# Optimization experiments

Measured on AMD Instinct MI355X. Metric: run time of the kernel, lower is better.

## Reference

```python
import jax, jax.numpy as jnp
import numpy as np

STEPS, BATCH = 2048, 512
INPUT_DIM = 16          # climate features after stripping flow channel
STORE_DIM = 8           # number of conceptual stores S
HIDDEN = 128
SLOW = 2                # SLOW_STORE index
RAIN_IDX = 0            # rain column within sliced climate inputs
OUT_DIM = STORE_DIM * (STORE_DIM + 2)   # flow_between_stores=True -> 80
IN_DIM_FLOWNET = INPUT_DIM + STORE_DIM  # 24


def setup_inputs() -> dict:
    key = jax.random.key(0)
    ks = jax.random.split(key, 10)
    hyd_input = jax.random.uniform(ks[0], (STEPS, BATCH, 1 + INPUT_DIM), dtype=jnp.float32)
    s = 0.05
    W0 = jax.random.normal(ks[1], (HIDDEN, IN_DIM_FLOWNET), dtype=jnp.float32) * s
    b0 = jax.random.normal(ks[2], (HIDDEN,), dtype=jnp.float32) * s
    W1 = jax.random.normal(ks[3], (HIDDEN, HIDDEN), dtype=jnp.float32) * s
    b1 = jax.random.normal(ks[4], (HIDDEN,), dtype=jnp.float32) * s
    W_in = jax.random.normal(ks[5], (STORE_DIM + 1, HIDDEN), dtype=jnp.float32) * s
    b_in = jax.random.normal(ks[6], (STORE_DIM + 1,), dtype=jnp.float32) * s
    W_out = jax.random.normal(ks[7], (OUT_DIM, HIDDEN), dtype=jnp.float32) * s
    b_out = jax.random.normal(ks[8], (OUT_DIM,), dtype=jnp.float32) * s - 3.0  # bias.data -= 3
    return {"hyd_input": hyd_input, "W0": W0, "b0": b0, "W1": W1, "b1": b1,
            "W_in": W_in, "b_in": b_in, "W_out": W_out, "b_out": b_out}


def reference(hyd_input, W0, b0, W1, b1, W_in, b_in, W_out, b_out):
    S = STORE_DIM
    flow = hyd_input[:, :, 0]          # [T, B] observed flow
    x = hyd_input[:, :, 1:]            # [T, B, F] climate forcings
    rain = x[:, :, RAIN_IDX]           # [T, B]
    # correct_init_baseflow: 25th percentile of observed flow over time, per batch elem
    baseflow = jnp.percentile(flow, 25.0, axis=0)  # [B]

    B = x.shape[1]
    stores0 = jnp.zeros((B, S), dtype=hyd_input.dtype).at[:, 1].set(1.0)  # init_stores

    def step(stores, inp):
        x_t, rain_t, is_first = inp
        # flownet: (num_layers=2) Linear -> ReLU (dropout is eval-mode identity)
        h = jnp.concatenate([x_t, 0.01 * stores], axis=1)      # [B, F+S]
        h = jax.nn.relu(h @ W0.T + b0)
        h = jax.nn.relu(h @ W1.T + b1)
        # inflow gating (softmax over S+1): distribute rain into stores
        a = jax.nn.softmax(h @ W_in.T + b_in, axis=-1)          # [B, S+1]
        stores = stores + a[:, 1:] * rain_t[:, None]
        # outflow fluxes (sigmoid), S*(S+2) = inter-store | escape | flow
        b = jax.nn.sigmoid(h @ W_out.T + b_out)                 # [B, S*(S+2)]
        # sequential inter-store transfers (order matters; S is small/fixed)
        for d in range(S):
            fb = b[:, d * S:(d + 1) * S] * stores               # [B, S]
            stores = (stores - fb).at[:, d].add(fb.sum(axis=1))
        escape = b[:, -2 * S:-S] * stores
        stores = stores - escape
        b_flow = b[:, -S:]
        flow_distn = b_flow * stores
        stores = stores - flow_distn
        # at i==0: overwrite slow store from baseflow / outflow coeff
        corrected = stores.at[:, SLOW].set(baseflow / jnp.maximum(b_flow[:, SLOW], 1e-5))
        stores = jnp.where(is_first, corrected, stores)
        return stores, flow_distn.sum(axis=1)

    is_first = jnp.arange(x.shape[0]) == 0
    _, flows = jax.lax.scan(step, stores0, (x, rain, is_first))
    return flows  # [T, B]
```

## Files before the change

### kernel.cpp

```cpp
#include <hip/hip_runtime.h>
#include <hip/hip_bf16.h>
#include <math.h>

#define STEPS 2048
#define BATCH 512

typedef __attribute__((ext_vector_type(8))) short short8;
typedef __attribute__((ext_vector_type(4))) short short4v;
typedef __attribute__((ext_vector_type(2))) short short2v;
typedef __attribute__((ext_vector_type(4))) float f32x4;
typedef __attribute__((ext_vector_type(2))) float f32x2;

__device__ __forceinline__ short f2bf(float f) {
    union { float f; unsigned u; } v; v.f = f;
    unsigned u = v.u;
    return (short)((u + 0x7FFFu + ((u >> 16) & 1u)) >> 16);
}
__device__ __forceinline__ short2v pk2(float a, float b) {
    __hip_bfloat162 h = __float22bfloat162_rn(make_float2(a, b));
    union { __hip_bfloat162 h; short2v s; } u; u.h = h; return u.s;
}

__global__ __launch_bounds__(256) void baseflow_kernel(
    const float* __restrict__ hyd, float* __restrict__ bf)
{
    __shared__ float arr[STEPS];
    const int b = blockIdx.x;
    const int tid = threadIdx.x;
    for (int t = tid; t < STEPS; t += 256)
        arr[t] = hyd[(size_t)(t * BATCH + b) * 17];
    __syncthreads();
    for (int k = 2; k <= STEPS; k <<= 1) {
        for (int j = k >> 1; j > 0; j >>= 1) {
            for (int i = tid; i < STEPS; i += 256) {
                int ixj = i ^ j;
                if (ixj > i) {
                    float a = arr[i], c = arr[ixj];
                    bool up = ((i & k) == 0);
                    if (up ? (a > c) : (a < c)) { arr[i] = c; arr[ixj] = a; }
                }
            }
            __syncthreads();
        }
    }
    if (tid == 0) bf[b] = arr[511] + 0.75f * (arr[512] - arr[511]);
}

__global__ __launch_bounds__(256, 1) void hyd_step_kernel(
    const float* __restrict__ hyd,
    const float* __restrict__ W0,  const float* __restrict__ b0,
    const float* __restrict__ W1,  const float* __restrict__ b1,
    const float* __restrict__ Win, const float* __restrict__ bin,
    const float* __restrict__ Wout,const float* __restrict__ bout,
    const float* __restrict__ baseflow,
    float* __restrict__ out)
{
    __shared__ __align__(16) short h1F[256 * 8];
    __shared__ __align__(16) short h2F[256 * 8];
    __shared__ __align__(16) float hb[2][100];

    const int tid  = threadIdx.x;
    const int blk  = blockIdx.x;
    const int lane = tid & 63;
    const int wv   = tid >> 6;
    const int cn   = lane & 15;
    const int cg   = lane >> 4;
    const int col  = lane & 1;

    for (int i = tid; i < 256 * 8; i += 256) { h1F[i] = 0; h2F[i] = 0; }

    short8 a0[2]; f32x4 c0[2];
    short8 a1[2][4]; f32x4 c1[2];
    short8 ah[2][4]; f32x4 ch[2];
    #pragma unroll
    for (int i = 0; i < 2; ++i) {
        const int mt = 2 * wv + i;
        const int row = mt * 16 + cn;
        #pragma unroll
        for (int j = 0; j < 8; ++j) {
            int k = cg * 8 + j;
            a0[i][j] = (k < 24) ? f2bf(W0[row * 24 + k]) : (short)0;
        }
        #pragma unroll
        for (int kt = 0; kt < 4; ++kt)
            #pragma unroll
            for (int j = 0; j < 8; ++j)
                a1[i][kt][j] = f2bf(W1[row * 128 + kt * 32 + cg * 8 + j]);
        #pragma unroll
        for (int r = 0; r < 4; ++r) {
            int m = mt * 16 + cg * 4 + r;
            c0[i][r] = b0[m];
            c1[i][r] = b1[m];
        }
    }
    const int nht = (wv < 2) ? 2 : 1;
    int htile[2];
    htile[0] = (wv < 2) ? 2 * wv : 4 + (wv - 2);
    htile[1] = (wv < 2) ? 2 * wv + 1 : htile[0];
    #pragma unroll
    for (int i = 0; i < 2; ++i) {
        const int ht = htile[i];
        const int row = ht * 16 + cn;
        #pragma unroll
        for (int kt = 0; kt < 4; ++kt)
            #pragma unroll
            for (int j = 0; j < 8; ++j) {
                int k = kt * 32 + cg * 8 + j;
                float w = 0.f;
                if (row != 1) {
                    int q = (row == 0) ? 0 : (row - 1);
                    if (q < 9)       w = Win[q * 128 + k];
                    else if (q < 89) w = Wout[(q - 9) * 128 + k];
                }
                ah[i][kt][j] = f2bf(w);
            }
        #pragma unroll
        for (int r = 0; r < 4; ++r) {
            int m = ht * 16 + cg * 4 + r;
            float bb = 0.f;
            if (m != 1) {
                int q = (m == 0) ? 0 : (m - 1);
                if (q < 9)       bb = bin[q];
                else if (q < 89) bb = bout[q - 9];
            }
            ch[i][r] = bb;
        }
    }

    f32x2 s01 = {0.f, 1.f}, s23 = {0.f, 0.f}, s45 = {0.f, 0.f}, s67 = {0.f, 0.f};
    const float bfv = baseflow[blk * 2 + col];
    short8 spack;
    {
        short2v p0 = pk2(0.01f * s01.x, 0.01f * s01.y);
        short2v p1 = pk2(0.01f * s23.x, 0.01f * s23.y);
        short2v p2 = pk2(0.01f * s45.x, 0.01f * s45.y);
        short2v p3 = pk2(0.01f * s67.x, 0.01f * s67.y);
        spack[0] = p0[0]; spack[1] = p0[1]; spack[2] = p1[0]; spack[3] = p1[1];
        spack[4] = p2[0]; spack[5] = p2[1]; spack[6] = p3[0]; spack[7] = p3[1];
    }

    const bool xlane = (cn < 2) && (cg < 2);
    const int xoff = (blk * 2 + cn) * 17 + 1 + cg * 8;
    const int roff = (blk * 2 + col) * 17 + 1;
    float xv[8];
    float rain_next;
    if (xlane) {
        const float* p = hyd + xoff;
        #pragma unroll
        for (int j = 0; j < 8; ++j) xv[j] = p[j];
    }
    rain_next = hyd[roff];

    f32x4 accx0, accx1;
    {
        short8 xfrag = 0;
        if (xlane) {
            short2v q0 = pk2(xv[0], xv[1]), q1 = pk2(xv[2], xv[3]),
                    q2 = pk2(xv[4], xv[5]), q3 = pk2(xv[6], xv[7]);
            xfrag[0] = q0[0]; xfrag[1] = q0[1]; xfrag[2] = q1[0]; xfrag[3] = q1[1];
            xfrag[4] = q2[0]; xfrag[5] = q2[1]; xfrag[6] = q3[0]; xfrag[7] = q3[1];
        }
        accx0 = __builtin_amdgcn_mfma_f32_16x16x32_bf16(a0[0], xfrag, c0[0], 0, 0, 0);
        accx1 = __builtin_amdgcn_mfma_f32_16x16x32_bf16(a0[1], xfrag, c0[1], 0, 0, 0);
    }

    __syncthreads();

    for (int t = 0; t < STEPS; ++t) {
        const float rain = rain_next;
        const int tn = (t + 1 < STEPS) ? (t + 1) : t;
        const float* px = hyd + (size_t)tn * (BATCH * 17);
        if (xlane) {
            const float* p = px + xoff;
            #pragma unroll
            for (int j = 0; j < 8; ++j) xv[j] = p[j];
        }
        rain_next = px[roff];

        short8 sfrag = 0;
        if (cn < 2 && cg == 2) sfrag = spack;
        #pragma unroll
        for (int i = 0; i < 2; ++i) {
            f32x4 acc = __builtin_amdgcn_mfma_f32_16x16x32_bf16(
                a0[i], sfrag, (i ? accx1 : accx0), 0, 0, 0);
            if (cn < 2) {
                int m0 = (2 * wv + i) * 16 + cg * 4;
                short4v p;
                short2v pa = pk2(fmaxf(acc[0], 0.f), fmaxf(acc[1], 0.f));
                short2v pb = pk2(fmaxf(acc[2], 0.f), fmaxf(acc[3], 0.f));
                p[0] = pa[0]; p[1] = pa[1]; p[2] = pb[0]; p[3] = pb[1];
                *(short4v*)&h1F[((m0 >> 3) * 16 + cn) * 8 + (m0 & 7)] = p;
            }
        }
        __syncthreads();

        short8 bf1[4];
        #pragma unroll
        for (int kt = 0; kt < 4; ++kt)
            bf1[kt] = *(const short8*)&h1F[(kt * 64 + lane) * 8];
        #pragma unroll
        for (int i = 0; i < 2; ++i) {
            f32x4 acc = c1[i];
            #pragma unroll
            for (int kt = 0; kt < 4; ++kt)
                acc = __builtin_amdgcn_mfma_f32_16x16x32_bf16(a1[i][kt], bf1[kt], acc, 0, 0, 0);
            if (cn < 2) {
                int m0 = (2 * wv + i) * 16 + cg * 4;
                short4v p;
                short2v pa = pk2(fmaxf(acc[0], 0.f), fmaxf(acc[1], 0.f));
                short2v pb = pk2(fmaxf(acc[2], 0.f), fmaxf(acc[3], 0.f));
                p[0] = pa[0]; p[1] = pa[1]; p[2] = pb[0]; p[3] = pb[1];
                *(short4v*)&h2F[((m0 >> 3) * 16 + cn) * 8 + (m0 & 7)] = p;
            }
        }
        __syncthreads();

        short8 bf2[4];
        #pragma unroll
        for (int kt = 0; kt < 4; ++kt)
            bf2[kt] = *(const short8*)&h2F[(kt * 64 + lane) * 8];
        #pragma unroll
        for (int i = 0; i < 2; ++i) {
            if (i < nht) {
                f32x4 acc = ch[i];
                #pragma unroll
                for (int kt = 0; kt < 4; ++kt)
                    acc = __builtin_amdgcn_mfma_f32_16x16x32_bf16(ah[i][kt], bf2[kt], acc, 0, 0, 0);
                if (cn < 2) {
                    const int ht = htile[i];
                    float4 o;
                    #pragma unroll
                    for (int r = 0; r < 4; ++r) {
                        int m = ht * 16 + cg * 4 + r;
                        float v = acc[r];
                        bool isl = (m < 10);
                        float em = __expf(isl ? v : -v);
                        float res = isl ? em : __builtin_amdgcn_rcpf(1.f + em);
                        ((float*)&o)[r] = res;
                    }
                    *(float4*)&hb[cn][ht * 16 + cg * 4] = o;
                }
            }
        }
        __syncthreads();

        float4 gq[23];
        {
            const float4* hp = (const float4*)&hb[col][0];
            #pragma unroll
            for (int c2 = 0; c2 < 23; ++c2) gq[c2] = hp[c2];
        }

        {
            short8 xfrag = 0;
            if (xlane) {
                short2v q0 = pk2(xv[0], xv[1]), q1 = pk2(xv[2], xv[3]),
                        q2 = pk2(xv[4], xv[5]), q3 = pk2(xv[6], xv[7]);
                xfrag[0] = q0[0]; xfrag[1] = q0[1]; xfrag[2] = q1[0]; xfrag[3] = q1[1];
                xfrag[4] = q2[0]; xfrag[5] = q2[1]; xfrag[6] = q3[0]; xfrag[7] = q3[1];
            }
            accx0 = __builtin_amdgcn_mfma_f32_16x16x32_bf16(a0[0], xfrag, c0[0], 0, 0, 0);
            accx1 = __builtin_amdgcn_mfma_f32_16x16x32_bf16(a0[1], xfrag, c0[1], 0, 0, 0);
        }

        {
            const f32x2* g2 = (const f32x2*)gq;
            const float* gv = (const float*)gq;

            f32x2 dt = (g2[1] + g2[2]) + (g2[3] + g2[4]);
            float den = gv[0] + dt.x + dt.y;
            float rr = rain * __builtin_amdgcn_rcpf(den);
            f32x2 rr2 = {rr, rr};
            s01 += g2[1] * rr2; s23 += g2[2] * rr2;
            s45 += g2[3] * rr2; s67 += g2[4] * rr2;

            #pragma unroll
            for (int d = 0; d < 8; ++d) {
                const int gb = 5 + 4 * d;
                f32x2 fb0 = g2[gb + 0] * s01, fb1 = g2[gb + 1] * s23;
                f32x2 fb2 = g2[gb + 2] * s45, fb3 = g2[gb + 3] * s67;
                f32x2 tt = (fb0 + fb1) + (fb2 + fb3);
                float fs = tt.x + tt.y;
                s01 -= fb0; s23 -= fb1; s45 -= fb2; s67 -= fb3;
                if      (d == 0) s01.x += fs;
                else if (d == 1) s01.y += fs;
                else if (d == 2) s23.x += fs;
                else if (d == 3) s23.y += fs;
                else if (d == 4) s45.x += fs;
                else if (d == 5) s45.y += fs;
                else if (d == 6) s67.x += fs;
                else             s67.y += fs;
            }
            s01 -= g2[37] * s01; s23 -= g2[38] * s23;
            s45 -= g2[39] * s45; s67 -= g2[40] * s67;
            f32x2 f0 = g2[41] * s01, f1 = g2[42] * s23;
            f32x2 f2 = g2[43] * s45, f3 = g2[44] * s67;
            f32x2 ft = (f0 + f1) + (f2 + f3);
            float fsum = ft.x + ft.y;
            s01 -= f0; s23 -= f1; s45 -= f2; s67 -= f3;
            if (t == 0) s23.x = bfv / fmaxf(gv[84], 1e-5f);

            {
                short2v p0 = pk2(0.01f * s01.x, 0.01f * s01.y);
                short2v p1 = pk2(0.01f * s23.x, 0.01f * s23.y);
                short2v p2 = pk2(0.01f * s45.x, 0.01f * s45.y);
                short2v p3 = pk2(0.01f * s67.x, 0.01f * s67.y);
                spack[0] = p0[0]; spack[1] = p0[1]; spack[2] = p1[0]; spack[3] = p1[1];
                spack[4] = p2[0]; spack[5] = p2[1]; spack[6] = p3[0]; spack[7] = p3[1];
            }
            if (tid < 2) out[(size_t)t * BATCH + blk * 2 + tid] = fsum;
        }
    }
}

extern "C" void kernel_launch(void* const* d_in, const int* in_sizes, int n_in,
                              void* d_out, int out_size, void* d_ws, size_t ws_size,
                              hipStream_t stream)
{
    const float* hyd  = (const float*)d_in[0];
    const float* W0   = (const float*)d_in[1];
    const float* b0   = (const float*)d_in[2];
    const float* W1   = (const float*)d_in[3];
    const float* b1   = (const float*)d_in[4];
    const float* Win  = (const float*)d_in[5];
    const float* bin  = (const float*)d_in[6];
    const float* Wout = (const float*)d_in[7];
    const float* bout = (const float*)d_in[8];
    float* out = (float*)d_out;
    float* bf  = (float*)d_ws;

    baseflow_kernel<<<BATCH, 256, 0, stream>>>(hyd, bf);
    hyd_step_kernel<<<BATCH / 2, 256, 0, stream>>>(
        hyd, W0, b0, W1, b1, Win, bin, Wout, bout, bf, out);
}
```

Baseline: 3.072 ms.

## Collapse recurrent step kernel to a single wavefront, dropping block barriers

The per-step MLP work for two batch elements moves from four wavefronts into one 64-lane wavefront that holds all weight fragments in registers. This removes the four __syncthreads per timestep, leaving only lgkmcnt waits on LDS. Biases move into LDS and are reloaded each step. The recurrent store update is split so its first half overlaps the second half's LDS loads. The cost is one wave doing all the MFMAs serially and much higher register pressure (all W1 and head tiles in VGPRs), which risks spills.

```diff
diff --git a/kernel.cpp b/kernel.cpp
--- a/kernel.cpp
+++ b/kernel.cpp
@@ -20,6 +20,9 @@
     __hip_bfloat162 h = __float22bfloat162_rn(make_float2(a, b));
     union { __hip_bfloat162 h; short2v s; } u; u.h = h; return u.s;
 }
+
+#define LGKM0()    asm volatile("s_waitcnt lgkmcnt(0)" ::: "memory")
+#define MEMFENCE() asm volatile("" ::: "memory")
 
 __global__ __launch_bounds__(256) void baseflow_kernel(
     const float* __restrict__ hyd, float* __restrict__ bf)
@@ -46,7 +49,7 @@
     if (tid == 0) bf[b] = arr[511] + 0.75f * (arr[512] - arr[511]);
 }
 
-__global__ __launch_bounds__(256, 1) void hyd_step_kernel(
+__global__ __launch_bounds__(64, 1) void hyd_step_kernel(
     const float* __restrict__ hyd,
     const float* __restrict__ W0,  const float* __restrict__ b0,
     const float* __restrict__ W1,  const float* __restrict__ b1,
@@ -55,76 +58,64 @@
     const float* __restrict__ baseflow,
     float* __restrict__ out)
 {
-    __shared__ __align__(16) short h1F[256 * 8];
-    __shared__ __align__(16) short h2F[256 * 8];
+    __shared__ __align__(16) short h1F[16 * 16 * 8];
+    __shared__ __align__(16) short h2F[16 * 16 * 8];
     __shared__ __align__(16) float hb[2][100];
-
-    const int tid  = threadIdx.x;
+    __shared__ __align__(16) float c0L[128];
+    __shared__ __align__(16) float c1L[128];
+    __shared__ __align__(16) float chL[96];
+
+    const int lane = threadIdx.x & 63;
     const int blk  = blockIdx.x;
-    const int lane = tid & 63;
-    const int wv   = tid >> 6;
     const int cn   = lane & 15;
     const int cg   = lane >> 4;
     const int col  = lane & 1;
 
-    for (int i = tid; i < 256 * 8; i += 256) { h1F[i] = 0; h2F[i] = 0; }
-
-    short8 a0[2]; f32x4 c0[2];
-    short8 a1[2][4]; f32x4 c1[2];
-    short8 ah[2][4]; f32x4 ch[2];
+    for (int i = lane; i < 16 * 16 * 8; i += 64) { h1F[i] = 0; h2F[i] = 0; }
+    for (int i = lane; i < 128; i += 64) { c0L[i] = b0[i]; c1L[i] = b1[i]; }
+    for (int i = lane; i < 96; i += 64) {
+        float v = 0.f;
+        if (i != 1) {
+            int q = (i == 0) ? 0 : (i - 1);
+            if (q < 9)       v = bin[q];
+            else if (q < 89) v = bout[q - 9];
+        }
+        chL[i] = v;
+    }
+
+    short8 a0[8];
+    short8 a1[8][4];
+    short8 ah[6][4];
     #pragma unroll
-    for (int i = 0; i < 2; ++i) {
-        const int mt = 2 * wv + i;
+    for (int mt = 0; mt < 8; ++mt) {
         const int row = mt * 16 + cn;
         #pragma unroll
         for (int j = 0; j < 8; ++j) {
             int k = cg * 8 + j;
-            a0[i][j] = (k < 24) ? f2bf(W0[row * 24 + k]) : (short)0;
+            a0[mt][j] = (k < 24) ? f2bf(W0[row * 24 + k]) : (short)0;
         }
         #pragma unroll
         for (int kt = 0; kt < 4; ++kt)
             #pragma unroll
             for (int j = 0; j < 8; ++j)
-                a1[i][kt][j] = f2bf(W1[row * 128 + kt * 32 + cg * 8 + j]);
-        #pragma unroll
-        for (int r = 0; r < 4; ++r) {
-            int m = mt * 16 + cg * 4 + r;
-            c0[i][r] = b0[m];
-            c1[i][r] = b1[m];
-        }
-    }
-    const int nht = (wv < 2) ? 2 : 1;
-    int htile[2];
-    htile[0] = (wv < 2) ? 2 * wv : 4 + (wv - 2);
-    htile[1] = (wv < 2) ? 2 * wv + 1 : htile[0];
+                a1[mt][kt][j] = f2bf(W1[row * 128 + kt * 32 + cg * 8 + j]);
+    }
     #pragma unroll
-    for (int i = 0; i < 2; ++i) {
-        const int ht = htile[i];
-        const int row = ht * 16 + cn;
+    for (int ht = 0; ht < 6; ++ht) {
+        const int p = ht * 16 + cn;
         #pragma unroll
         for (int kt = 0; kt < 4; ++kt)
             #pragma unroll
             for (int j = 0; j < 8; ++j) {
                 int k = kt * 32 + cg * 8 + j;
                 float w = 0.f;
-                if (row != 1) {
-                    int q = (row == 0) ? 0 : (row - 1);
+                if (p != 1) {
+                    int q = (p == 0) ? 0 : (p - 1);
                     if (q < 9)       w = Win[q * 128 + k];
                     else if (q < 89) w = Wout[(q - 9) * 128 + k];
                 }
-                ah[i][kt][j] = f2bf(w);
-            }
-        #pragma unroll
-        for (int r = 0; r < 4; ++r) {
-            int m = ht * 16 + cg * 4 + r;
-            float bb = 0.f;
-            if (m != 1) {
-                int q = (m == 0) ? 0 : (m - 1);
-                if (q < 9)       bb = bin[q];
-                else if (q < 89) bb = bout[q - 9];
-            }
-            ch[i][r] = bb;
-        }
+                ah[ht][kt][j] = f2bf(w);
+            }
     }
 
     f32x2 s01 = {0.f, 1.f}, s23 = {0.f, 0.f}, s45 = {0.f, 0.f}, s67 = {0.f, 0.f};
@@ -151,7 +142,11 @@
     }
     rain_next = hyd[roff];
 
-    f32x4 accx0, accx1;
+    const int wbase = ((cg >> 1) * 16 + cn) * 8 + (cg & 1) * 4;
+
+    LGKM0();
+
+    f32x4 accx[8];
     {
         short8 xfrag = 0;
         if (xlane) {
@@ -160,11 +155,12 @@
             xfrag[0] = q0[0]; xfrag[1] = q0[1]; xfrag[2] = q1[0]; xfrag[3] = q1[1];
             xfrag[4] = q2[0]; xfrag[5] = q2[1]; xfrag[6] = q3[0]; xfrag[7] = q3[1];
         }
-        accx0 = __builtin_amdgcn_mfma_f32_16x16x32_bf16(a0[0], xfrag, c0[0], 0, 0, 0);
-        accx1 = __builtin_amdgcn_mfma_f32_16x16x32_bf16(a0[1], xfrag, c0[1], 0, 0, 0);
-    }
-
-    __syncthreads();
+        #pragma unroll
+        for (int mt = 0; mt < 8; ++mt) {
+            f32x4 c0v = *(const f32x4*)&c0L[mt * 16 + cg * 4];
+            accx[mt] = __builtin_amdgcn_mfma_f32_16x16x32_bf16(a0[mt], xfrag, c0v, 0, 0, 0);
+        }
+    }
 
     for (int t = 0; t < STEPS; ++t) {
         const float rain = rain_next;
@@ -180,77 +176,83 @@
         short8 sfrag = 0;
         if (cn < 2 && cg == 2) sfrag = spack;
         #pragma unroll
-        for (int i = 0; i < 2; ++i) {
-            f32x4 acc = __builtin_amdgcn_mfma_f32_16x16x32_bf16(
-                a0[i], sfrag, (i ? accx1 : accx0), 0, 0, 0);
+        for (int mt = 0; mt < 8; ++mt) {
+            f32x4 acc = __builtin_amdgcn_mfma_f32_16x16x32_bf16(a0[mt], sfrag, accx[mt], 0, 0, 0);
             if (cn < 2) {
-                int m0 = (2 * wv + i) * 16 + cg * 4;
                 short4v p;
                 short2v pa = pk2(fmaxf(acc[0], 0.f), fmaxf(acc[1], 0.f));
                 short2v pb = pk2(fmaxf(acc[2], 0.f), fmaxf(acc[3], 0.f));
                 p[0] = pa[0]; p[1] = pa[1]; p[2] = pb[0]; p[3] = pb[1];
-                *(short4v*)&h1F[((m0 >> 3) * 16 + cn) * 8 + (m0 & 7)] = p;
-            }
-        }
-        __syncthreads();
+                *(short4v*)&h1F[wbase + mt * 256] = p;
+            }
+        }
+        f32x4 c1v[8];
+        #pragma unroll
+        for (int mt = 0; mt < 8; ++mt)
+            c1v[mt] = *(const f32x4*)&c1L[mt * 16 + cg * 4];
+        LGKM0();
 
         short8 bf1[4];
         #pragma unroll
         for (int kt = 0; kt < 4; ++kt)
             bf1[kt] = *(const short8*)&h1F[(kt * 64 + lane) * 8];
-        #pragma unroll
-        for (int i = 0; i < 2; ++i) {
-            f32x4 acc = c1[i];
+        f32x4 chv[6];
+        #pragma unroll
+        for (int ht = 0; ht < 6; ++ht)
+            chv[ht] = *(const f32x4*)&chL[ht * 16 + cg * 4];
+        #pragma unroll
+        for (int mt = 0; mt < 8; ++mt) {
+            f32x4 acc = c1v[mt];
             #pragma unroll
             for (int kt = 0; kt < 4; ++kt)
-                acc = __builtin_amdgcn_mfma_f32_16x16x32_bf16(a1[i][kt], bf1[kt], acc, 0, 0, 0);
+                acc = __builtin_amdgcn_mfma_f32_16x16x32_bf16(a1[mt][kt], bf1[kt], acc, 0, 0, 0);
             if (cn < 2) {
-                int m0 = (2 * wv + i) * 16 + cg * 4;
                 short4v p;
                 short2v pa = pk2(fmaxf(acc[0], 0.f), fmaxf(acc[1], 0.f));
                 short2v pb = pk2(fmaxf(acc[2], 0.f), fmaxf(acc[3], 0.f));
                 p[0] = pa[0]; p[1] = pa[1]; p[2] = pb[0]; p[3] = pb[1];
-                *(short4v*)&h2F[((m0 >> 3) * 16 + cn) * 8 + (m0 & 7)] = p;
-            }
-        }
-        __syncthreads();
+                *(short4v*)&h2F[wbase + mt * 256] = p;
+            }
+        }
+        LGKM0();
 
         short8 bf2[4];
         #pragma unroll
         for (int kt = 0; kt < 4; ++kt)
             bf2[kt] = *(const short8*)&h2F[(kt * 64 + lane) * 8];
         #pragma unroll
-        for (int i = 0; i < 2; ++i) {
-            if (i < nht) {
-                f32x4 acc = ch[i];
-                #pragma unroll
-                for (int kt = 0; kt < 4; ++kt)
-                    acc = __builtin_amdgcn_mfma_f32_16x16x32_bf16(ah[i][kt], bf2[kt], acc, 0, 0, 0);
-                if (cn < 2) {
-                    const int ht = htile[i];
-                    float4 o;
+        for (int ht = 0; ht < 6; ++ht) {
+            f32x4 acc = chv[ht];
+            #pragma unroll
+            for (int kt = 0; kt < 4; ++kt)
+                acc = __builtin_amdgcn_mfma_f32_16x16x32_bf16(ah[ht][kt], bf2[kt], acc, 0, 0, 0);
+            if (cn < 2) {
+                f32x4 o;
+                if (ht == 0) {
                     #pragma unroll
                     for (int r = 0; r < 4; ++r) {
-                        int m = ht * 16 + cg * 4 + r;
+                        int m = cg * 4 + r;
                         float v = acc[r];
                         bool isl = (m < 10);
                         float em = __expf(isl ? v : -v);
-                        float res = isl ? em : __builtin_amdgcn_rcpf(1.f + em);
-                        ((float*)&o)[r] = res;
+                        o[r] = isl ? em : __builtin_amdgcn_rcpf(1.f + em);
                     }
-                    *(float4*)&hb[cn][ht * 16 + cg * 4] = o;
+                } else {
+                    #pragma unroll
+                    for (int r = 0; r < 4; ++r) {
+                        float em = __expf(-acc[r]);
+                        o[r] = __builtin_amdgcn_rcpf(1.f + em);
+                    }
                 }
-            }
-        }
-        __syncthreads();
-
-        float4 gq[23];
-        {
-            const float4* hp = (const float4*)&hb[col][0];
-            #pragma unroll
-            for (int c2 = 0; c2 < 23; ++c2) gq[c2] = hp[c2];
-        }
-
+                *(f32x4*)&hb[cn][ht * 16 + cg * 4] = o;
+            }
+        }
+        LGKM0();
+
+        f32x4 gqA[11];
+        #pragma unroll
+        for (int c2 = 0; c2 < 11; ++c2)
+            gqA[c2] = *(const f32x4*)&hb[col][c2 * 4];
         {
             short8 xfrag = 0;
             if (xlane) {
@@ -259,46 +261,68 @@
                 xfrag[0] = q0[0]; xfrag[1] = q0[1]; xfrag[2] = q1[0]; xfrag[3] = q1[1];
                 xfrag[4] = q2[0]; xfrag[5] = q2[1]; xfrag[6] = q3[0]; xfrag[7] = q3[1];
             }
-            accx0 = __builtin_amdgcn_mfma_f32_16x16x32_bf16(a0[0], xfrag, c0[0], 0, 0, 0);
-            accx1 = __builtin_amdgcn_mfma_f32_16x16x32_bf16(a0[1], xfrag, c0[1], 0, 0, 0);
-        }
-
+            #pragma unroll
+            for (int mt = 0; mt < 8; ++mt) {
+                f32x4 c0v = *(const f32x4*)&c0L[mt * 16 + cg * 4];
+                accx[mt] = __builtin_amdgcn_mfma_f32_16x16x32_bf16(a0[mt], xfrag, c0v, 0, 0, 0);
+            }
+        }
+
+        const float* gvA = (const float*)gqA;
+        const f32x2* gA2 = (const f32x2*)gqA;
         {
-            const f32x2* g2 = (const f32x2*)gq;
-            const float* gv = (const float*)gq;
-
-            f32x2 dt = (g2[1] + g2[2]) + (g2[3] + g2[4]);
-            float den = gv[0] + dt.x + dt.y;
+            f32x2 dt = (gA2[1] + gA2[2]) + (gA2[3] + gA2[4]);
+            float den = gvA[0] + dt.x + dt.y;
             float rr = rain * __builtin_amdgcn_rcpf(den);
             f32x2 rr2 = {rr, rr};
-            s01 += g2[1] * rr2; s23 += g2[2] * rr2;
-            s45 += g2[3] * rr2; s67 += g2[4] * rr2;
-
-            #pragma unroll
-            for (int d = 0; d < 8; ++d) {
+            s01 += gA2[1] * rr2; s23 += gA2[2] * rr2;
+            s45 += gA2[3] * rr2; s67 += gA2[4] * rr2;
+
+            #pragma unroll
+            for (int d = 0; d < 4; ++d) {
                 const int gb = 5 + 4 * d;
-                f32x2 fb0 = g2[gb + 0] * s01, fb1 = g2[gb + 1] * s23;
-                f32x2 fb2 = g2[gb + 2] * s45, fb3 = g2[gb + 3] * s67;
+                f32x2 fb0 = gA2[gb + 0] * s01, fb1 = gA2[gb + 1] * s23;
+                f32x2 fb2 = gA2[gb + 2] * s45, fb3 = gA2[gb + 3] * s67;
                 f32x2 tt = (fb0 + fb1) + (fb2 + fb3);
                 float fs = tt.x + tt.y;
                 s01 -= fb0; s23 -= fb1; s45 -= fb2; s67 -= fb3;
                 if      (d == 0) s01.x += fs;
                 else if (d == 1) s01.y += fs;
                 else if (d == 2) s23.x += fs;
-                else if (d == 3) s23.y += fs;
-                else if (d == 4) s45.x += fs;
+                else             s23.y += fs;
+            }
+        }
+
+        MEMFENCE();
+
+        f32x4 gqB[13];
+        #pragma unroll
+        for (int c2 = 0; c2 < 13; ++c2)
+            gqB[c2] = *(const f32x4*)&hb[col][40 + c2 * 4];
+        const float* gvB = (const float*)gqB;
+        const f32x2* gB2 = (const f32x2*)gqB;
+        {
+            #pragma unroll
+            for (int d = 4; d < 8; ++d) {
+                const int gb = 4 * d - 15;
+                f32x2 fb0 = gB2[gb + 0] * s01, fb1 = gB2[gb + 1] * s23;
+                f32x2 fb2 = gB2[gb + 2] * s45, fb3 = gB2[gb + 3] * s67;
+                f32x2 tt = (fb0 + fb1) + (fb2 + fb3);
+                float fs = tt.x + tt.y;
+                s01 -= fb0; s23 -= fb1; s45 -= fb2; s67 -= fb3;
+                if      (d == 4) s45.x += fs;
                 else if (d == 5) s45.y += fs;
                 else if (d == 6) s67.x += fs;
                 else             s67.y += fs;
             }
-            s01 -= g2[37] * s01; s23 -= g2[38] * s23;
-            s45 -= g2[39] * s45; s67 -= g2[40] * s67;
-            f32x2 f0 = g2[41] * s01, f1 = g2[42] * s23;
-            f32x2 f2 = g2[43] * s45, f3 = g2[44] * s67;
+            s01 -= gB2[17] * s01; s23 -= gB2[18] * s23;
+            s45 -= gB2[19] * s45; s67 -= gB2[20] * s67;
+            f32x2 f0 = gB2[21] * s01, f1 = gB2[22] * s23;
+            f32x2 f2 = gB2[23] * s45, f3 = gB2[24] * s67;
             f32x2 ft = (f0 + f1) + (f2 + f3);
             float fsum = ft.x + ft.y;
             s01 -= f0; s23 -= f1; s45 -= f2; s67 -= f3;
-            if (t == 0) s23.x = bfv / fmaxf(gv[84], 1e-5f);
+            if (t == 0) s23.x = bfv / fmaxf(gvB[44], 1e-5f);
 
             {
                 short2v p0 = pk2(0.01f * s01.x, 0.01f * s01.y);
@@ -308,7 +332,7 @@
                 spack[0] = p0[0]; spack[1] = p0[1]; spack[2] = p1[0]; spack[3] = p1[1];
                 spack[4] = p2[0]; spack[5] = p2[1]; spack[6] = p3[0]; spack[7] = p3[1];
             }
-            if (tid < 2) out[(size_t)t * BATCH + blk * 2 + tid] = fsum;
+            if (lane < 2) out[(size_t)t * BATCH + blk * 2 + lane] = fsum;
         }
     }
 }
@@ -330,6 +354,6 @@
     float* bf  = (float*)d_ws;
 
     baseflow_kernel<<<BATCH, 256, 0, stream>>>(hyd, bf);
-    hyd_step_kernel<<<BATCH / 2, 256, 0, stream>>>(
+    hyd_step_kernel<<<BATCH / 2, 64, 0, stream>>>(
         hyd, W0, b0, W1, b1, Win, bin, Wout, bout, bf, out);
 }
```

New measurement: 5.538 ms. +80.3%, slower.

## Use LDS-only barriers, split MFMA accumulation chains, and stage gate loads

Applied to the files above, without the earlier changes.

Replaces __syncthreads with a barrier that waits only on LDS counters, so the global prefetch of the next step's inputs is not drained at each barrier. The dependent 4-MFMA accumulation chains are split into two independent pairs that are summed afterwards, which shortens MFMA latency chains. Gate values are loaded from LDS in two batches, interleaved with the first half of the store-transfer loop, and the sigmoid/exp branch is specialised by tile. This lowers register pressure and latency, but a barrier that skips vmcnt could be fragile if any global memory ordering were relied upon.

```diff
diff --git a/kernel.cpp b/kernel.cpp
--- a/kernel.cpp
+++ b/kernel.cpp
@@ -20,6 +20,10 @@
     __hip_bfloat162 h = __float22bfloat162_rn(make_float2(a, b));
     union { __hip_bfloat162 h; short2v s; } u; u.h = h; return u.s;
 }
+
+#define LBAR() do { asm volatile("s_waitcnt lgkmcnt(0)" ::: "memory"); \
+                    __builtin_amdgcn_s_barrier();                      \
+                    asm volatile("" ::: "memory"); } while (0)
 
 __global__ __launch_bounds__(256) void baseflow_kernel(
     const float* __restrict__ hyd, float* __restrict__ bf)
@@ -164,8 +168,6 @@
         accx1 = __builtin_amdgcn_mfma_f32_16x16x32_bf16(a0[1], xfrag, c0[1], 0, 0, 0);
     }
 
-    __syncthreads();
-
     for (int t = 0; t < STEPS; ++t) {
         const float rain = rain_next;
         const int tn = (t + 1 < STEPS) ? (t + 1) : t;
@@ -192,7 +194,7 @@
                 *(short4v*)&h1F[((m0 >> 3) * 16 + cn) * 8 + (m0 & 7)] = p;
             }
         }
-        __syncthreads();
+        LBAR();
 
         short8 bf1[4];
         #pragma unroll
@@ -200,10 +202,12 @@
             bf1[kt] = *(const short8*)&h1F[(kt * 64 + lane) * 8];
         #pragma unroll
         for (int i = 0; i < 2; ++i) {
-            f32x4 acc = c1[i];
-            #pragma unroll
-            for (int kt = 0; kt < 4; ++kt)
-                acc = __builtin_amdgcn_mfma_f32_16x16x32_bf16(a1[i][kt], bf1[kt], acc, 0, 0, 0);
+            f32x4 zz = {0.f, 0.f, 0.f, 0.f};
+            f32x4 accA = __builtin_amdgcn_mfma_f32_16x16x32_bf16(a1[i][0], bf1[0], c1[i], 0, 0, 0);
+            accA = __builtin_amdgcn_mfma_f32_16x16x32_bf16(a1[i][1], bf1[1], accA, 0, 0, 0);
+            f32x4 accB = __builtin_amdgcn_mfma_f32_16x16x32_bf16(a1[i][2], bf1[2], zz, 0, 0, 0);
+            accB = __builtin_amdgcn_mfma_f32_16x16x32_bf16(a1[i][3], bf1[3], accB, 0, 0, 0);
+            f32x4 acc = accA + accB;
             if (cn < 2) {
                 int m0 = (2 * wv + i) * 16 + cg * 4;
                 short4v p;
@@ -213,7 +217,7 @@
                 *(short4v*)&h2F[((m0 >> 3) * 16 + cn) * 8 + (m0 & 7)] = p;
             }
         }
-        __syncthreads();
+        LBAR();
 
         short8 bf2[4];
         #pragma unroll
@@ -222,35 +226,41 @@
         #pragma unroll
         for (int i = 0; i < 2; ++i) {
             if (i < nht) {
-                f32x4 acc = ch[i];
-                #pragma unroll
-                for (int kt = 0; kt < 4; ++kt)
-                    acc = __builtin_amdgcn_mfma_f32_16x16x32_bf16(ah[i][kt], bf2[kt], acc, 0, 0, 0);
+                f32x4 zz = {0.f, 0.f, 0.f, 0.f};
+                f32x4 accA = __builtin_amdgcn_mfma_f32_16x16x32_bf16(ah[i][0], bf2[0], ch[i], 0, 0, 0);
+                accA = __builtin_amdgcn_mfma_f32_16x16x32_bf16(ah[i][1], bf2[1], accA, 0, 0, 0);
+                f32x4 accB = __builtin_amdgcn_mfma_f32_16x16x32_bf16(ah[i][2], bf2[2], zz, 0, 0, 0);
+                accB = __builtin_amdgcn_mfma_f32_16x16x32_bf16(ah[i][3], bf2[3], accB, 0, 0, 0);
+                f32x4 acc = accA + accB;
                 if (cn < 2) {
                     const int ht = htile[i];
-                    float4 o;
-                    #pragma unroll
-                    for (int r = 0; r < 4; ++r) {
-                        int m = ht * 16 + cg * 4 + r;
-                        float v = acc[r];
-                        bool isl = (m < 10);
-                        float em = __expf(isl ? v : -v);
-                        float res = isl ? em : __builtin_amdgcn_rcpf(1.f + em);
-                        ((float*)&o)[r] = res;
+                    f32x4 o;
+                    if (ht == 0) {
+                        #pragma unroll
+                        for (int r = 0; r < 4; ++r) {
+                            int m = cg * 4 + r;
+                            float v = acc[r];
+                            bool isl = (m < 10);
+                            float em = __expf(isl ? v : -v);
+                            o[r] = isl ? em : __builtin_amdgcn_rcpf(1.f + em);
+                        }
+                    } else {
+                        #pragma unroll
+                        for (int r = 0; r < 4; ++r) {
+                            float em = __expf(-acc[r]);
+                            o[r] = __builtin_amdgcn_rcpf(1.f + em);
+                        }
                     }
-                    *(float4*)&hb[cn][ht * 16 + cg * 4] = o;
+                    *(f32x4*)&hb[cn][ht * 16 + cg * 4] = o;
                 }
             }
         }
-        __syncthreads();
-
-        float4 gq[23];
-        {
-            const float4* hp = (const float4*)&hb[col][0];
-            #pragma unroll
-            for (int c2 = 0; c2 < 23; ++c2) gq[c2] = hp[c2];
-        }
-
+        LBAR();
+
+        f32x4 gqA[11];
+        #pragma unroll
+        for (int c2 = 0; c2 < 11; ++c2)
+            gqA[c2] = *(const f32x4*)&hb[col][c2 * 4];
         {
             short8 xfrag = 0;
             if (xlane) {
@@ -263,42 +273,59 @@
             accx1 = __builtin_amdgcn_mfma_f32_16x16x32_bf16(a0[1], xfrag, c0[1], 0, 0, 0);
         }
 
+        const float* gvA = (const float*)gqA;
+        const f32x2* gA2 = (const f32x2*)gqA;
         {
-            const f32x2* g2 = (const f32x2*)gq;
-            const float* gv = (const float*)gq;
-
-            f32x2 dt = (g2[1] + g2[2]) + (g2[3] + g2[4]);
-            float den = gv[0] + dt.x + dt.y;
+            f32x2 dt = (gA2[1] + gA2[2]) + (gA2[3] + gA2[4]);
+            float den = gvA[0] + dt.x + dt.y;
             float rr = rain * __builtin_amdgcn_rcpf(den);
             f32x2 rr2 = {rr, rr};
-            s01 += g2[1] * rr2; s23 += g2[2] * rr2;
-            s45 += g2[3] * rr2; s67 += g2[4] * rr2;
-
-            #pragma unroll
-            for (int d = 0; d < 8; ++d) {
+            s01 += gA2[1] * rr2; s23 += gA2[2] * rr2;
+            s45 += gA2[3] * rr2; s67 += gA2[4] * rr2;
+
+            #pragma unroll
+            for (int d = 0; d < 4; ++d) {
                 const int gb = 5 + 4 * d;
-                f32x2 fb0 = g2[gb + 0] * s01, fb1 = g2[gb + 1] * s23;
-                f32x2 fb2 = g2[gb + 2] * s45, fb3 = g2[gb + 3] * s67;
+                f32x2 fb0 = gA2[gb + 0] * s01, fb1 = gA2[gb + 1] * s23;
+                f32x2 fb2 = gA2[gb + 2] * s45, fb3 = gA2[gb + 3] * s67;
                 f32x2 tt = (fb0 + fb1) + (fb2 + fb3);
                 float fs = tt.x + tt.y;
                 s01 -= fb0; s23 -= fb1; s45 -= fb2; s67 -= fb3;
                 if      (d == 0) s01.x += fs;
                 else if (d == 1) s01.y += fs;
                 else if (d == 2) s23.x += fs;
-                else if (d == 3) s23.y += fs;
-                else if (d == 4) s45.x += fs;
+                else             s23.y += fs;
+            }
+        }
+
+        f32x4 gqB[13];
+        #pragma unroll
+        for (int c2 = 0; c2 < 13; ++c2)
+            gqB[c2] = *(const f32x4*)&hb[col][40 + c2 * 4];
+        const float* gvB = (const float*)gqB;
+        const f32x2* gB2 = (const f32x2*)gqB;
+        {
+            #pragma unroll
+            for (int d = 4; d < 8; ++d) {
+                const int gb = 4 * d - 15;
+                f32x2 fb0 = gB2[gb + 0] * s01, fb1 = gB2[gb + 1] * s23;
+                f32x2 fb2 = gB2[gb + 2] * s45, fb3 = gB2[gb + 3] * s67;
+                f32x2 tt = (fb0 + fb1) + (fb2 + fb3);
+                float fs = tt.x + tt.y;
+                s01 -= fb0; s23 -= fb1; s45 -= fb2; s67 -= fb3;
+                if      (d == 4) s45.x += fs;
                 else if (d == 5) s45.y += fs;
                 else if (d == 6) s67.x += fs;
                 else             s67.y += fs;
             }
-            s01 -= g2[37] * s01; s23 -= g2[38] * s23;
-            s45 -= g2[39] * s45; s67 -= g2[40] * s67;
-            f32x2 f0 = g2[41] * s01, f1 = g2[42] * s23;
-            f32x2 f2 = g2[43] * s45, f3 = g2[44] * s67;
+            s01 -= gB2[17] * s01; s23 -= gB2[18] * s23;
+            s45 -= gB2[19] * s45; s67 -= gB2[20] * s67;
+            f32x2 f0 = gB2[21] * s01, f1 = gB2[22] * s23;
+            f32x2 f2 = gB2[23] * s45, f3 = gB2[24] * s67;
             f32x2 ft = (f0 + f1) + (f2 + f3);
             float fsum = ft.x + ft.y;
             s01 -= f0; s23 -= f1; s45 -= f2; s67 -= f3;
-            if (t == 0) s23.x = bfv / fmaxf(gv[84], 1e-5f);
+            if (t == 0) s23.x = bfv / fmaxf(gvB[44], 1e-5f);
 
             {
                 short2v p0 = pk2(0.01f * s01.x, 0.01f * s01.y);
```

Result: faster. 2.935 ms (-4.4%).
